# Kernel tuning notes

Hardware: AMD Instinct MI355X
Metric: run time of the kernel (lower is better)

## Reference

```python
import jax, jax.numpy as jnp
import numpy as np

B = 32
NEG_INF = -1e30


def _conv2d(x, w, b):
    # x: (B,C,H,W), w: (O,I,kh,kw), VALID, stride 1
    y = jax.lax.conv_general_dilated(x, w, (1, 1), 'VALID',
                                     dimension_numbers=('NCHW', 'OIHW', 'NCHW'))
    return y + b[None, :, None, None]


def _maxpool_3_2_1(x):
    return jax.lax.reduce_window(x, NEG_INF, jax.lax.max,
                                 (1, 1, 3, 3), (1, 1, 2, 2),
                                 ((0, 0), (0, 0), (1, 1), (1, 1)))


def _extract_patches(x, kh, kw, stride):
    # x: (B,C,H,W) -> (B,C,oh,kh,ow,kw)
    H, W = x.shape[2], x.shape[3]
    oh = (H - kh) // stride + 1
    ow = (W - kw) // stride + 1
    rows = jnp.arange(oh)[:, None] * stride + jnp.arange(kh)[None, :]  # (oh,kh)
    cols = jnp.arange(ow)[:, None] * stride + jnp.arange(kw)[None, :]  # (ow,kw)
    return x[:, :, rows][:, :, :, :, cols]  # (B,C,oh,kh,ow,kw)


def _local_conv(x, w, b, stride):
    # unshared-weight conv. w: (oh,ow,oc,ic,kh,kw), b: (oc,oh,ow)
    kh, kw = w.shape[4], w.shape[5]
    p = _extract_patches(x, kh, kw, stride)              # (B,ic,oh,kh,ow,kw)
    y = jnp.einsum('bcpkql,pqockl->bopq', p, w)          # (B,oc,oh,ow)
    return y + b[None]


def setup_inputs() -> dict:
    key = jax.random.key(0)
    ks = jax.random.split(key, 14)
    s = 0.05
    f32 = jnp.float32
    inp = {
        'x': jax.random.normal(ks[0], (B, 3, 152, 152), dtype=f32),
        'conv1_w': jax.random.normal(ks[1], (32, 3, 11, 11), dtype=f32) * s,
        'conv1_b': jax.random.normal(ks[2], (32,), dtype=f32) * s,
        'conv2_w': jax.random.normal(ks[3], (16, 32, 9, 9), dtype=f32) * s,
        'conv2_b': jax.random.normal(ks[4], (16,), dtype=f32) * s,
        'lc1_w': jax.random.normal(ks[5], (55, 55, 16, 16, 9, 9), dtype=f32) * s,
        'lc1_b': jax.random.normal(ks[6], (16, 55, 55), dtype=f32) * s,
        'lc2_w': jax.random.normal(ks[7], (25, 25, 16, 16, 7, 7), dtype=f32) * s,
        'lc2_b': jax.random.normal(ks[8], (16, 25, 25), dtype=f32) * s,
        'lc3_w': jax.random.normal(ks[9], (21, 21, 16, 16, 5, 5), dtype=f32) * s,
        'lc3_b': jax.random.normal(ks[10], (16, 21, 21), dtype=f32) * s,
        'fc1_w': jax.random.normal(ks[11], (4096, 16 * 21 * 21), dtype=f32) * s,
        'fc1_b': jax.random.normal(ks[12], (4096,), dtype=f32) * s,
    }
    return inp


def reference(x, conv1_w, conv1_b, conv2_w, conv2_b,
              lc1_w, lc1_b, lc2_w, lc2_b, lc3_w, lc3_b,
              fc1_w, fc1_b):
    h = jax.nn.relu(_conv2d(x, conv1_w, conv1_b))        # (B,32,142,142)
    h = _maxpool_3_2_1(h)                                # (B,32,71,71)
    h = jax.nn.relu(_conv2d(h, conv2_w, conv2_b))        # (B,16,63,63)
    h = jax.nn.relu(_local_conv(h, lc1_w, lc1_b, 1))     # (B,16,55,55)
    h = jax.nn.relu(_local_conv(h, lc2_w, lc2_b, 2))     # (B,16,25,25)
    h = jax.nn.relu(_local_conv(h, lc3_w, lc3_b, 1))     # (B,16,21,21)
    h = h.reshape(h.shape[0], 16 * 21 * 21)
    return h @ fc1_w.T + fc1_b                           # (B,4096)
```

## Files before the change

kernel.cpp:

```cpp
#include <hip/hip_runtime.h>
#include <cstddef>

typedef __attribute__((ext_vector_type(8))) short bf16x8;
typedef __attribute__((ext_vector_type(8), aligned(8))) short bf16x8a;
typedef __attribute__((ext_vector_type(4))) float f32x4;
typedef __attribute__((ext_vector_type(4))) unsigned short u16x4;
typedef __attribute__((ext_vector_type(8))) unsigned short u16x8;

__device__ inline unsigned short f2bf(float f) {
  unsigned int u = __float_as_uint(f);
  unsigned int r = (u + 0x7FFFu + ((u >> 16) & 1u)) >> 16;
  return (unsigned short)r;
}
__device__ inline float bf2f(unsigned short u) {
  return __uint_as_float((unsigned int)u << 16);
}

__global__ __launch_bounds__(256) void prep_x1w1(const float* __restrict__ x,
                                                 const float* __restrict__ w,
                                                 unsigned short* __restrict__ xb,
                                                 unsigned short* __restrict__ wb) {
  if (blockIdx.x < 3040) {
    const int j = blockIdx.x * 256 + threadIdx.x;
    const int iw = j % 160;
    const int ih = (j / 160) % 152;
    const int b = j / (160 * 152);
    unsigned short v[4] = {0, 0, 0, 0};
    if (iw < 152) {
      #pragma unroll
      for (int ic = 0; ic < 3; ++ic)
        v[ic] = f2bf(x[(size_t)(b * 3 + ic) * 23104 + ih * 152 + iw]);
    }
    *(unsigned long long*)(xb + ((((size_t)ih * 160 + iw) * 32) + b) * 4) =
        *(unsigned long long*)v;
  } else {
    const int j = (blockIdx.x - 3040) * 256 + threadIdx.x;
    const int e = j & 7;
    const int s = (j >> 3) & 31;
    const int kcj = j >> 8;
    const int kc = kcj & 3, step = kcj >> 2;
    const int t = step * 8 + kc * 2 + (e >> 2);
    const int ics = e & 3;
    const int kh = t / 12, kwp = t - kh * 12;
    float val = 0.f;
    if (t < 132 && kwp < 11 && ics < 3)
      val = w[((s * 3 + ics) * 11 + kh) * 11 + kwp];
    wb[j] = f2bf(val);
  }
}

__global__ __launch_bounds__(256, 4) void conv1_mfma(const unsigned short* __restrict__ xb,
                                                     const unsigned short* __restrict__ wb,
                                                     const float* __restrict__ bias,
                                                     unsigned short* __restrict__ outB) {
  const int lane = threadIdx.x & 63;
  const int wvi = threadIdx.x >> 6;
  const int pos = blockIdx.x * 4 + wvi;
  const int oh = pos / 142, ow = pos % 142;
  const int row = lane & 15;
  const int kc = lane >> 4;
  f32x4 a00 = {0.f, 0.f, 0.f, 0.f}, a01 = a00, a10 = a00, a11 = a00;

  #pragma unroll 2
  for (int j = 0; j < 17; ++j) {
    const int t0 = j * 8 + 2 * kc;
    int kh = t0 / 12;
    int kwp = t0 - kh * 12;
    if (t0 >= 132) { kh = 0; kwp = 0; }
    const bf16x8 wa0 = *(const bf16x8*)(wb + (((j * 4 + kc) * 32) + row) * 8);
    const bf16x8 wa1 = *(const bf16x8*)(wb + (((j * 4 + kc) * 32) + 16 + row) * 8);
    const size_t base = (((size_t)(oh + kh) * 160) + (ow + kwp)) * 128;
    const unsigned short* xp0 = xb + base + row * 4;
    bf16x8 xv0, xv1;
    ((unsigned long long*)&xv0)[0] = *(const unsigned long long*)(xp0);
    ((unsigned long long*)&xv0)[1] = *(const unsigned long long*)(xp0 + 128);
    ((unsigned long long*)&xv1)[0] = *(const unsigned long long*)(xp0 + 64);
    ((unsigned long long*)&xv1)[1] = *(const unsigned long long*)(xp0 + 192);
    a00 = __builtin_amdgcn_mfma_f32_16x16x32_bf16(wa0, xv0, a00, 0, 0, 0);
    a01 = __builtin_amdgcn_mfma_f32_16x16x32_bf16(wa0, xv1, a01, 0, 0, 0);
    a10 = __builtin_amdgcn_mfma_f32_16x16x32_bf16(wa1, xv0, a10, 0, 0, 0);
    a11 = __builtin_amdgcn_mfma_f32_16x16x32_bf16(wa1, xv1, a11, 0, 0, 0);
  }

  unsigned short* ob = outB + (size_t)pos * 1024;
  u16x4 p00, p01, p10, p11;
  #pragma unroll
  for (int r = 0; r < 4; ++r) {
    const float bv0 = bias[kc * 4 + r];
    const float bv1 = bias[16 + kc * 4 + r];
    p00[r] = f2bf(fmaxf(a00[r] + bv0, 0.f));
    p01[r] = f2bf(fmaxf(a01[r] + bv0, 0.f));
    p10[r] = f2bf(fmaxf(a10[r] + bv1, 0.f));
    p11[r] = f2bf(fmaxf(a11[r] + bv1, 0.f));
  }
  *(u16x4*)(ob + row * 32 + kc * 4) = p00;
  *(u16x4*)(ob + (row + 16) * 32 + kc * 4) = p01;
  *(u16x4*)(ob + row * 32 + 16 + kc * 4) = p10;
  *(u16x4*)(ob + (row + 16) * 32 + 16 + kc * 4) = p11;
}

__global__ __launch_bounds__(256) void poolt2_wb2(const unsigned short* __restrict__ in,
                                                  unsigned short* __restrict__ xb,
                                                  const float* __restrict__ w2,
                                                  unsigned short* __restrict__ wb2) {
  if (blockIdx.x < 631) {
    const int tid = threadIdx.x;
    const int b = tid & 31, pg = tid >> 5;
    const int posp = blockIdx.x * 8 + pg;
    if (posp >= 5041) return;
    const int ohp = posp / 71, owp = posp % 71;
    u16x8 m[4];
    #pragma unroll
    for (int q = 0; q < 4; ++q)
      #pragma unroll
      for (int e = 0; e < 8; ++e) m[q][e] = 0;

    #pragma unroll
    for (int kh = 0; kh < 3; ++kh) {
      const int ih = ohp * 2 - 1 + kh;
      if (ih < 0 || ih >= 142) continue;
      #pragma unroll
      for (int kw = 0; kw < 3; ++kw) {
        const int iw = owp * 2 - 1 + kw;
        if (iw < 0 || iw >= 142) continue;
        const u16x8* p =
            (const u16x8*)(in + (((size_t)(ih * 142 + iw)) * 32 + b) * 32);
        #pragma unroll
        for (int q = 0; q < 4; ++q) {
          const u16x8 v = p[q];
          #pragma unroll
          for (int e = 0; e < 8; ++e) m[q][e] = (v[e] > m[q][e]) ? v[e] : m[q][e];
        }
      }
    }
    u16x8* o = (u16x8*)(xb + ((size_t)posp * 32 + b) * 32);
    #pragma unroll
    for (int q = 0; q < 4; ++q) o[q] = m[q];
  } else {
    const int j = (blockIdx.x - 631) * 256 + threadIdx.x;
    const int ic = j & 31, oc = (j >> 5) & 15, sp = j >> 9;
    wb2[j] = f2bf(w2[(size_t)oc * 2592 + ic * 81 + sp]);
  }
}

__global__ __launch_bounds__(256) void conv2_mfma(const unsigned short* __restrict__ xb,
                                                  const unsigned short* __restrict__ wb,
                                                  const float* __restrict__ bias,
                                                  unsigned short* __restrict__ outB) {
  const int lane = threadIdx.x & 63;
  const int wvi = threadIdx.x >> 6;
  int pos = blockIdx.x * 4 + wvi;
  if (pos > 3968) pos = 3968;
  const int oh = pos / 63, ow = pos % 63;
  const int row = lane & 15;
  const int kc = lane >> 4;
  f32x4 acc0 = {0.f, 0.f, 0.f, 0.f}, acc1 = {0.f, 0.f, 0.f, 0.f};
  const unsigned short* xbase = xb + (size_t)(oh * 71 + ow) * 1024;
  const int aoff = row * 32 + kc * 8;
  const int boff0 = aoff;
  const int boff1 = (row + 16) * 32 + kc * 8;

  #pragma unroll
  for (int g = 0; g < 20; ++g) {
    bf16x8 A[4], Ba[4], Bb[4];
    #pragma unroll
    for (int i = 0; i < 4; ++i) {
      const int sp = g * 4 + i;
      const int kh = sp / 9, kw = sp - kh * 9;
      A[i] = *(const bf16x8*)(wb + sp * 512 + aoff);
      const unsigned short* xp = xbase + (kh * 71 + kw) * 1024;
      Ba[i] = *(const bf16x8*)(xp + boff0);
      Bb[i] = *(const bf16x8*)(xp + boff1);
    }
    #pragma unroll
    for (int i = 0; i < 4; ++i) {
      acc0 = __builtin_amdgcn_mfma_f32_16x16x32_bf16(A[i], Ba[i], acc0, 0, 0, 0);
      acc1 = __builtin_amdgcn_mfma_f32_16x16x32_bf16(A[i], Bb[i], acc1, 0, 0, 0);
    }
  }
  {
    const bf16x8 a = *(const bf16x8*)(wb + 80 * 512 + aoff);
    const unsigned short* xp = xbase + (8 * 71 + 8) * 1024;
    const bf16x8 b0 = *(const bf16x8*)(xp + boff0);
    const bf16x8 b1 = *(const bf16x8*)(xp + boff1);
    acc0 = __builtin_amdgcn_mfma_f32_16x16x32_bf16(a, b0, acc0, 0, 0, 0);
    acc1 = __builtin_amdgcn_mfma_f32_16x16x32_bf16(a, b1, acc1, 0, 0, 0);
  }

  u16x4 pk0, pk1;
  #pragma unroll
  for (int r = 0; r < 4; ++r) {
    const float bv = bias[kc * 4 + r];
    pk0[r] = f2bf(fmaxf(acc0[r] + bv, 0.f));
    pk1[r] = f2bf(fmaxf(acc1[r] + bv, 0.f));
  }
  *(u16x4*)(outB + (size_t)pos * 512 + row * 16 + kc * 4) = pk0;
  *(u16x4*)(outB + (size_t)pos * 512 + (row + 16) * 16 + kc * 4) = pk1;
}

__global__ __launch_bounds__(256) void prep_lcw_all(const float* __restrict__ w1,
                                                    unsigned short* __restrict__ o1,
                                                    const float* __restrict__ w2,
                                                    unsigned short* __restrict__ o2,
                                                    const float* __restrict__ w3,
                                                    unsigned short* __restrict__ o3) {
  __shared__ float ls[8 * 16 * 81];
  int blk = blockIdx.x;
  const float* wp;
  unsigned short* ob;
  int KHW;
  if (blk < 3025) {
    KHW = 81; wp = w1 + (size_t)blk * 256 * 81; ob = o1 + (size_t)blk * 41 * 512;
  } else if (blk < 3650) {
    blk -= 3025;
    KHW = 49; wp = w2 + (size_t)blk * 256 * 49; ob = o2 + (size_t)blk * 25 * 512;
  } else {
    blk -= 3650;
    KHW = 25; wp = w3 + (size_t)blk * 256 * 25; ob = o3 + (size_t)blk * 13 * 512;
  }
  const int P = (KHW + 1) / 2;
  const int tid = threadIdx.x;

  for (int half = 0; half < 2; ++half) {
    __syncthreads();
    for (int j = tid; j < 8 * 16 * KHW; j += 256)
      ls[j] = wp[half * (8 * 16 * KHW) + j];
    __syncthreads();
    for (int j = tid; j < P * 256; j += 256) {
      const int ic = j & 15, tl = (j >> 4) & 1, oc8 = (j >> 5) & 7, pair = j >> 8;
      const int tap = pair * 2 + tl;
      const float v = (tap < KHW) ? ls[(oc8 * 16 + ic) * KHW + tap] : 0.f;
      ob[(size_t)pair * 512 + (half * 8 + oc8) * 32 + tl * 16 + ic] = f2bf(v);
    }
  }
}

template <int KH, int S, int IH, int OH>
__global__ __launch_bounds__(256) void lc_mfma(const unsigned short* __restrict__ xb,
                                               const unsigned short* __restrict__ wbT,
                                               const float* __restrict__ bias,
                                               unsigned short* __restrict__ out,
                                               int pos_count) {
  constexpr int KHW = KH * KH;
  constexpr int P = (KHW + 1) / 2;
  constexpr int NPOS = OH * OH;
  const int lane = threadIdx.x & 63;
  const int wvi = threadIdx.x >> 6;
  int lpos = blockIdx.x * 4 + wvi;
  if (lpos >= pos_count) lpos = pos_count - 1;
  const int pos = lpos;
  const int oh = pos / OH, ow = pos % OH;
  const int bcol = lane & 15;
  const int kc = lane >> 4;
  const int tsel = kc >> 1;
  const int icoff = (kc & 1) * 8;
  f32x4 acc0 = {0.f, 0.f, 0.f, 0.f}, acc1 = {0.f, 0.f, 0.f, 0.f};
  const unsigned short* wp = wbT + (size_t)lpos * (P * 512) + bcol * 32 + kc * 8;
  const int xorg = (oh * S) * IH + ow * S;

  #pragma unroll
  for (int g = 0; g < P / 4; ++g) {
    bf16x8 A[4], Ba[4], Bb[4];
    #pragma unroll
    for (int i = 0; i < 4; ++i) {
      const int p = g * 4 + i;
      const int t0 = 2 * p, t1 = 2 * p + 1;
      const int o0 = (t0 / KH) * IH + (t0 % KH);
      const int o1 = (t1 / KH) * IH + (t1 % KH);
      const int osel = tsel ? o1 : o0;
      A[i] = *(const bf16x8*)(wp + p * 512);
      const unsigned short* xp = xb + (size_t)(xorg + osel) * 512 + icoff;
      Ba[i] = *(const bf16x8*)(xp + bcol * 16);
      Bb[i] = *(const bf16x8*)(xp + (bcol + 16) * 16);
    }
    #pragma unroll
    for (int i = 0; i < 4; ++i) {
      acc0 = __builtin_amdgcn_mfma_f32_16x16x32_bf16(A[i], Ba[i], acc0, 0, 0, 0);
      acc1 = __builtin_amdgcn_mfma_f32_16x16x32_bf16(A[i], Bb[i], acc1, 0, 0, 0);
    }
  }
  {
    constexpr int p = P - 1;
    const int t0 = 2 * p;
    const int o0 = (t0 / KH) * IH + (t0 % KH);
    const bf16x8 a = *(const bf16x8*)(wp + p * 512);
    const unsigned short* xp = xb + (size_t)(xorg + o0) * 512 + icoff;
    const bf16x8 b0 = *(const bf16x8*)(xp + bcol * 16);
    const bf16x8 b1 = *(const bf16x8*)(xp + (bcol + 16) * 16);
    acc0 = __builtin_amdgcn_mfma_f32_16x16x32_bf16(a, b0, acc0, 0, 0, 0);
    acc1 = __builtin_amdgcn_mfma_f32_16x16x32_bf16(a, b1, acc1, 0, 0, 0);
  }

  u16x4 pk0, pk1;
  #pragma unroll
  for (int r = 0; r < 4; ++r) {
    const float bv = bias[(kc * 4 + r) * NPOS + pos];
    pk0[r] = f2bf(fmaxf(acc0[r] + bv, 0.f));
    pk1[r] = f2bf(fmaxf(acc1[r] + bv, 0.f));
  }
  *(u16x4*)(out + (size_t)pos * 512 + bcol * 16 + kc * 4) = pk0;
  *(u16x4*)(out + (size_t)pos * 512 + (bcol + 16) * 16 + kc * 4) = pk1;
}

__global__ __launch_bounds__(256) void fc_reformat2(const unsigned short* __restrict__ xb5,
                                                    float* __restrict__ xB) {
  const int j = blockIdx.x * 256 + threadIdx.x;
  const int k = j % 7056;
  const int b = j / 7056;
  const int oc = k / 441, pos = k % 441;
  xB[j] = bf2f(xb5[((size_t)pos * 32 + b) * 16 + oc]);
}

__global__ __launch_bounds__(256) void fc1_v5(const float* __restrict__ xB,
                                              const float* __restrict__ w,
                                              float* __restrict__ part) {
  const int lane = threadIdx.x & 63;
  const int b0 = (threadIdx.x >> 6) * 8;
  const int n0 = blockIdx.x * 8;
  const int kch = blockIdx.y;
  const int kbase = kch * 1764;
  float acc[8][8] = {};
  for (int it = 0; it < 7; ++it) {
    const int ko = it * 256 + lane * 4;
    const int kb = kbase + ko;
    float4 wf[8], xr[8];
    if (ko < 1764) {
      #pragma unroll
      for (int n = 0; n < 8; ++n)
        wf[n] = *(const float4*)&w[(size_t)(n0 + n) * 7056 + kb];
      #pragma unroll
      for (int bb = 0; bb < 8; ++bb)
        xr[bb] = *(const float4*)&xB[(size_t)(b0 + bb) * 7056 + kb];
    } else {
      #pragma unroll
      for (int n = 0; n < 8; ++n) wf[n] = make_float4(0.f, 0.f, 0.f, 0.f);
      #pragma unroll
      for (int bb = 0; bb < 8; ++bb) xr[bb] = make_float4(0.f, 0.f, 0.f, 0.f);
    }
    #pragma unroll
    for (int n = 0; n < 8; ++n)
      #pragma unroll
      for (int bb = 0; bb < 8; ++bb) {
        acc[n][bb] += wf[n].x * xr[bb].x + wf[n].y * xr[bb].y +
                      wf[n].z * xr[bb].z + wf[n].w * xr[bb].w;
      }
  }
  #pragma unroll
  for (int n = 0; n < 8; ++n)
    #pragma unroll
    for (int c = 0; c < 8; ++c)
      #pragma unroll
      for (int m = 1; m < 64; m <<= 1)
        acc[n][c] += __shfl_xor(acc[n][c], m, 64);
  float val = 0.f;
  #pragma unroll
  for (int n = 0; n < 8; ++n)
    #pragma unroll
    for (int c = 0; c < 8; ++c)
      if (lane == n * 8 + c) val = acc[n][c];
  const int n_l = lane >> 3, b_l = lane & 7;
  part[(((size_t)kch * 4096 + n0 + n_l) * 32) + b0 + b_l] = val;
}

__global__ __launch_bounds__(256) void fc_combine(const float* __restrict__ part,
                                                  const float* __restrict__ bias,
                                                  float* __restrict__ out) {
  const int j = blockIdx.x * 256 + threadIdx.x;
  const int n = j & 4095, b = j >> 12;
  float v = bias[n];
  #pragma unroll
  for (int k = 0; k < 4; ++k) v += part[(((size_t)k * 4096 + n) * 32) + b];
  out[(size_t)b * 4096 + n] = v;
}

extern "C" void kernel_launch(void* const* d_in, const int* in_sizes, int n_in,
                              void* d_out, int out_size, void* d_ws, size_t ws_size,
                              hipStream_t stream) {
  const float* x       = (const float*)d_in[0];
  const float* conv1_w = (const float*)d_in[1];
  const float* conv1_b = (const float*)d_in[2];
  const float* conv2_w = (const float*)d_in[3];
  const float* conv2_b = (const float*)d_in[4];
  const float* lc1_w   = (const float*)d_in[5];
  const float* lc1_b   = (const float*)d_in[6];
  const float* lc2_w   = (const float*)d_in[7];
  const float* lc2_b   = (const float*)d_in[8];
  const float* lc3_w   = (const float*)d_in[9];
  const float* lc3_b   = (const float*)d_in[10];
  const float* fc1_w   = (const float*)d_in[11];
  const float* fc1_b   = (const float*)d_in[12];
  float* out = (float*)d_out;
  char* ws = (char*)d_ws;

  unsigned short* xb1  = (unsigned short*)(ws + 0);
  unsigned short* wb1  = (unsigned short*)(ws + 8388608);
  unsigned short* c1B  = (unsigned short*)(ws + 16777216);
  unsigned short* xb2  = (unsigned short*)(ws + 67108864);
  unsigned short* wb2  = (unsigned short*)(ws + 83886080);
  unsigned short* h2b  = (unsigned short*)(ws + 92274688);
  unsigned short* xb3  = (unsigned short*)(ws + 100663296);
  unsigned short* xb4  = (unsigned short*)(ws + 109051904);
  unsigned short* xb5  = (unsigned short*)(ws + 117440512);
  float* xB            = (float*)(ws + 125829120);
  float* fcp           = (float*)(ws + 134217728);
  unsigned short* wbT1 = (unsigned short*)(ws + 167772160);
  unsigned short* wbT2 = (unsigned short*)(ws + 301989888);
  unsigned short* wbT3 = (unsigned short*)(ws + 318767104);

  prep_x1w1<<<3108, 256, 0, stream>>>(x, conv1_w, xb1, wb1);
  conv1_mfma<<<5041, 256, 0, stream>>>(xb1, wb1, conv1_b, c1B);
  poolt2_wb2<<<793, 256, 0, stream>>>(c1B, xb2, conv2_w, wb2);
  conv2_mfma<<<993, 256, 0, stream>>>(xb2, wb2, conv2_b, h2b);

  prep_lcw_all<<<4091, 256, 0, stream>>>(lc1_w, wbT1, lc2_w, wbT2, lc3_w, wbT3);
  lc_mfma<9, 1, 63, 55><<<757, 256, 0, stream>>>(h2b, wbT1, lc1_b, xb3, 3025);
  lc_mfma<7, 2, 55, 25><<<157, 256, 0, stream>>>(xb3, wbT2, lc2_b, xb4, 625);
  lc_mfma<5, 1, 25, 21><<<111, 256, 0, stream>>>(xb4, wbT3, lc3_b, xb5, 441);

  fc_reformat2<<<882, 256, 0, stream>>>(xb5, xB);
  fc1_v5<<<dim3(512, 4), 256, 0, stream>>>(xB, fc1_w, fcp);
  fc_combine<<<512, 256, 0, stream>>>(fcp, fc1_b, out);
}
```

Before: 379.3 us.

## Stage conv1 input tile in LDS and compute two output columns per wave

conv1 now launches a 2D grid where each block handles one output row and 8 output columns. The block first cooperatively loads an 11x19-pixel input window into shared memory, then each wave computes two output positions from LDS instead of global memory. This reuses overlapping input pixels across neighbouring columns and loads each weight fragment once per two positions. In exchange it adds a barrier, about 53 KB of LDS per block (limiting occupancy), and some redundant work where the last tile is clamped to overlap the previous one.

```diff
diff --git a/kernel.cpp b/kernel.cpp
--- a/kernel.cpp
+++ b/kernel.cpp
@@ -49,17 +49,33 @@
   }
 }
 
-__global__ __launch_bounds__(256, 4) void conv1_mfma(const unsigned short* __restrict__ xb,
-                                                     const unsigned short* __restrict__ wb,
-                                                     const float* __restrict__ bias,
-                                                     unsigned short* __restrict__ outB) {
-  const int lane = threadIdx.x & 63;
-  const int wvi = threadIdx.x >> 6;
-  const int pos = blockIdx.x * 4 + wvi;
-  const int oh = pos / 142, ow = pos % 142;
+__global__ __launch_bounds__(256) void conv1_mfma(const unsigned short* __restrict__ xb,
+                                                  const unsigned short* __restrict__ wb,
+                                                  const float* __restrict__ bias,
+                                                  unsigned short* __restrict__ outB) {
+  __shared__ unsigned short xs[11 * 19 * 128];
+  const int tile = blockIdx.x;
+  const int oh = blockIdx.y;
+  const int ow0 = min(tile * 8, 134);
+  const int tid = threadIdx.x;
+
+  for (int ch = tid; ch < 3344; ch += 256) {
+    const int e = ch & 15;
+    const int pix = ch >> 4;
+    const int c = pix % 19, r = pix / 19;
+    *(u16x8*)(xs + (size_t)pix * 128 + e * 8) =
+        *(const u16x8*)(xb + (((size_t)(oh + r) * 160) + (ow0 + c)) * 128 + e * 8);
+  }
+  __syncthreads();
+
+  const int lane = tid & 63, wvi = tid >> 6;
   const int row = lane & 15;
   const int kc = lane >> 4;
-  f32x4 a00 = {0.f, 0.f, 0.f, 0.f}, a01 = a00, a10 = a00, a11 = a00;
+  f32x4 acc[2][4];
+  #pragma unroll
+  for (int p = 0; p < 2; ++p)
+    #pragma unroll
+    for (int q = 0; q < 4; ++q) acc[p][q] = (f32x4){0.f, 0.f, 0.f, 0.f};
 
   #pragma unroll 2
   for (int j = 0; j < 17; ++j) {
@@ -69,34 +85,41 @@
     if (t0 >= 132) { kh = 0; kwp = 0; }
     const bf16x8 wa0 = *(const bf16x8*)(wb + (((j * 4 + kc) * 32) + row) * 8);
     const bf16x8 wa1 = *(const bf16x8*)(wb + (((j * 4 + kc) * 32) + 16 + row) * 8);
-    const size_t base = (((size_t)(oh + kh) * 160) + (ow + kwp)) * 128;
-    const unsigned short* xp0 = xb + base + row * 4;
-    bf16x8 xv0, xv1;
-    ((unsigned long long*)&xv0)[0] = *(const unsigned long long*)(xp0);
-    ((unsigned long long*)&xv0)[1] = *(const unsigned long long*)(xp0 + 128);
-    ((unsigned long long*)&xv1)[0] = *(const unsigned long long*)(xp0 + 64);
-    ((unsigned long long*)&xv1)[1] = *(const unsigned long long*)(xp0 + 192);
-    a00 = __builtin_amdgcn_mfma_f32_16x16x32_bf16(wa0, xv0, a00, 0, 0, 0);
-    a01 = __builtin_amdgcn_mfma_f32_16x16x32_bf16(wa0, xv1, a01, 0, 0, 0);
-    a10 = __builtin_amdgcn_mfma_f32_16x16x32_bf16(wa1, xv0, a10, 0, 0, 0);
-    a11 = __builtin_amdgcn_mfma_f32_16x16x32_bf16(wa1, xv1, a11, 0, 0, 0);
-  }
-
-  unsigned short* ob = outB + (size_t)pos * 1024;
-  u16x4 p00, p01, p10, p11;
-  #pragma unroll
-  for (int r = 0; r < 4; ++r) {
-    const float bv0 = bias[kc * 4 + r];
-    const float bv1 = bias[16 + kc * 4 + r];
-    p00[r] = f2bf(fmaxf(a00[r] + bv0, 0.f));
-    p01[r] = f2bf(fmaxf(a01[r] + bv0, 0.f));
-    p10[r] = f2bf(fmaxf(a10[r] + bv1, 0.f));
-    p11[r] = f2bf(fmaxf(a11[r] + bv1, 0.f));
-  }
-  *(u16x4*)(ob + row * 32 + kc * 4) = p00;
-  *(u16x4*)(ob + (row + 16) * 32 + kc * 4) = p01;
-  *(u16x4*)(ob + row * 32 + 16 + kc * 4) = p10;
-  *(u16x4*)(ob + (row + 16) * 32 + 16 + kc * 4) = p11;
+    #pragma unroll
+    for (int p = 0; p < 2; ++p) {
+      const int cl = wvi + p * 4 + kwp;
+      const unsigned short* xp = xs + (kh * 19 + cl) * 128 + row * 4;
+      bf16x8 xv0, xv1;
+      ((unsigned long long*)&xv0)[0] = *(const unsigned long long*)(xp);
+      ((unsigned long long*)&xv0)[1] = *(const unsigned long long*)(xp + 128);
+      ((unsigned long long*)&xv1)[0] = *(const unsigned long long*)(xp + 64);
+      ((unsigned long long*)&xv1)[1] = *(const unsigned long long*)(xp + 192);
+      acc[p][0] = __builtin_amdgcn_mfma_f32_16x16x32_bf16(wa0, xv0, acc[p][0], 0, 0, 0);
+      acc[p][1] = __builtin_amdgcn_mfma_f32_16x16x32_bf16(wa0, xv1, acc[p][1], 0, 0, 0);
+      acc[p][2] = __builtin_amdgcn_mfma_f32_16x16x32_bf16(wa1, xv0, acc[p][2], 0, 0, 0);
+      acc[p][3] = __builtin_amdgcn_mfma_f32_16x16x32_bf16(wa1, xv1, acc[p][3], 0, 0, 0);
+    }
+  }
+
+  #pragma unroll
+  for (int p = 0; p < 2; ++p) {
+    const int pos = oh * 142 + ow0 + wvi + p * 4;
+    unsigned short* ob = outB + (size_t)pos * 1024;
+    u16x4 p00, p01, p10, p11;
+    #pragma unroll
+    for (int r = 0; r < 4; ++r) {
+      const float bv0 = bias[kc * 4 + r];
+      const float bv1 = bias[16 + kc * 4 + r];
+      p00[r] = f2bf(fmaxf(acc[p][0][r] + bv0, 0.f));
+      p01[r] = f2bf(fmaxf(acc[p][1][r] + bv0, 0.f));
+      p10[r] = f2bf(fmaxf(acc[p][2][r] + bv1, 0.f));
+      p11[r] = f2bf(fmaxf(acc[p][3][r] + bv1, 0.f));
+    }
+    *(u16x4*)(ob + row * 32 + kc * 4) = p00;
+    *(u16x4*)(ob + (row + 16) * 32 + kc * 4) = p01;
+    *(u16x4*)(ob + row * 32 + 16 + kc * 4) = p10;
+    *(u16x4*)(ob + (row + 16) * 32 + 16 + kc * 4) = p11;
+  }
 }
 
 __global__ __launch_bounds__(256) void poolt2_wb2(const unsigned short* __restrict__ in,
@@ -408,7 +431,7 @@
   unsigned short* wbT3 = (unsigned short*)(ws + 318767104);
 
   prep_x1w1<<<3108, 256, 0, stream>>>(x, conv1_w, xb1, wb1);
-  conv1_mfma<<<5041, 256, 0, stream>>>(xb1, wb1, conv1_b, c1B);
+  conv1_mfma<<<dim3(18, 142), 256, 0, stream>>>(xb1, wb1, conv1_b, c1B);
   poolt2_wb2<<<793, 256, 0, stream>>>(c1B, xb2, conv2_w, wb2);
   conv2_mfma<<<993, 256, 0, stream>>>(xb2, wb2, conv2_b, h2b);
 
```

After: 352.5 us. 7.1% less time.
